# Kernel tuning notes

Measured on AMD Instinct MI355X. Metric: run time of the kernel, lower is better.

Reference implementation:

```python
import jax, jax.numpy as jnp
import numpy as np

N_NODES = 10000
N_EDGES = 80000
IN_DIM = 512
H1, H2, OUT_DIM = 4096, 1024, 7
NEG_SLOPE = 0.2


def _gat_layer(x, src, dst, W, a_src, a_dst, b, n_nodes):
    # x: [N, F_in] -> h: [N, F_out]
    h = x @ W
    # per-edge attention logits: a_src . h_i + a_dst . h_j (PyG GATConv, heads=1)
    e = jax.nn.leaky_relu((h @ a_src)[src] + (h @ a_dst)[dst], NEG_SLOPE)
    # segment softmax over destination nodes
    m = jax.ops.segment_max(e, dst, num_segments=n_nodes)
    ex = jnp.exp(e - m[dst])
    denom = jax.ops.segment_sum(ex, dst, num_segments=n_nodes)
    alpha = ex / denom[dst]
    # scatter-add weighted messages
    out = jax.ops.segment_sum(alpha[:, None] * h[src], dst, num_segments=n_nodes)
    return out + b


def setup_inputs() -> dict:
    key = jax.random.key(0)
    ks = jax.random.split(key, 16)
    s = 0.05
    inp = {
        "x": jax.random.normal(ks[0], (N_NODES, IN_DIM), dtype=jnp.float32),
        "edge_index": jax.random.randint(ks[1], (2, N_EDGES), 0, N_NODES, dtype=jnp.int32),
        "W1": jax.random.normal(ks[2], (IN_DIM, H1), dtype=jnp.float32) * s,
        "att_src1": jax.random.normal(ks[3], (H1,), dtype=jnp.float32) * s,
        "att_dst1": jax.random.normal(ks[4], (H1,), dtype=jnp.float32) * s,
        "b1": jnp.zeros((H1,), dtype=jnp.float32),
        "W2": jax.random.normal(ks[5], (H1, H2), dtype=jnp.float32) * s,
        "att_src2": jax.random.normal(ks[6], (H2,), dtype=jnp.float32) * s,
        "att_dst2": jax.random.normal(ks[7], (H2,), dtype=jnp.float32) * s,
        "b2": jnp.zeros((H2,), dtype=jnp.float32),
        "W3": jax.random.normal(ks[8], (H2, OUT_DIM), dtype=jnp.float32) * s,
        "att_src3": jax.random.normal(ks[9], (OUT_DIM,), dtype=jnp.float32) * s,
        "att_dst3": jax.random.normal(ks[10], (OUT_DIM,), dtype=jnp.float32) * s,
        "b3": jnp.zeros((OUT_DIM,), dtype=jnp.float32),
    }
    return inp


def reference(x, edge_index, W1, att_src1, att_dst1, b1,
              W2, att_src2, att_dst2, b2,
              W3, att_src3, att_dst3, b3):
    n = x.shape[0]
    loops = jnp.arange(n, dtype=edge_index.dtype)
    src = jnp.concatenate([edge_index[0], loops])  # add_self_loops=True
    dst = jnp.concatenate([edge_index[1], loops])
    h = _gat_layer(x, src, dst, W1, att_src1, att_dst1, b1, n)
    h = jax.nn.relu(h)  # dropout is identity in eval mode
    h = _gat_layer(h, src, dst, W2, att_src2, att_dst2, b2, n)
    h = jax.nn.relu(h)
    h = _gat_layer(h, src, dst, W3, att_src3, att_dst3, b3, n)
    return jax.nn.log_softmax(h, axis=1)
```

## Files before the change

### kernel.cpp

```cpp
#include <hip/hip_runtime.h>
#include <hip/hip_bf16.h>
#include <math.h>

#define NNODES  10000
#define NEDGES  80000
#define NTOT    90000
#define IN_DIM  512
#define H1_DIM  4096
#define H2_DIM  1024
#define ODIM    7
#define MAXDEG  128
#define NEG_SLOPE 0.2f
#define MROWS   10240
#define NBX1    (H1_DIM / 128)

typedef __hip_bfloat16 bf16;
typedef __attribute__((ext_vector_type(8))) short short8;
typedef __attribute__((ext_vector_type(4))) float f32x4;

__device__ inline void unpack_bf2(unsigned u, float& lo, float& hi) {
    union { unsigned i; float f; } a, b;
    a.i = u << 16; b.i = u & 0xffff0000u;
    lo = a.f; hi = b.f;
}

#define ASYNC_COPY16(lds, g)                                                              \
    __builtin_amdgcn_global_load_lds((const __attribute__((address_space(1))) void*)(g),  \
                                     (__attribute__((address_space(3))) void*)(lds),      \
                                     16, 0, 0)

__global__ __launch_bounds__(256) void prep_all(const float* __restrict__ W1,
                                                bf16* __restrict__ W1T,
                                                const float* __restrict__ as1,
                                                const float* __restrict__ ad1,
                                                float* __restrict__ w1s,
                                                float* __restrict__ w1d,
                                                const float* __restrict__ W2,
                                                bf16* __restrict__ W2T,
                                                const float* __restrict__ as2,
                                                const float* __restrict__ ad2,
                                                float* __restrict__ w2s,
                                                float* __restrict__ w2d,
                                                const int* __restrict__ ei,
                                                int* cnt, int* bucket) {
    const int nb1 = (H1_DIM / 32) * (IN_DIM / 32);
    const int nb2 = (H2_DIM / 32) * (H1_DIM / 32);
    int bid = blockIdx.x;

    if (bid >= nb1 + nb2) {
        int k = (bid - nb1 - nb2) * 256 + threadIdx.x;
        if (k < NTOT) {
            int s, d;
            if (k < NEDGES) { s = ei[k]; d = ei[NEDGES + k]; }
            else            { s = k - NEDGES; d = s; }
            int pos = atomicAdd(&cnt[d], 1);
            if (pos < MAXDEG) bucket[d * MAXDEG + pos] = s;
        }
        return;
    }

    const float *W, *a_s, *a_d; bf16 *WT; float *w_s, *w_d; int R, C, cblocks;
    if (bid < nb1) { W = W1; WT = W1T; a_s = as1; a_d = ad1; w_s = w1s; w_d = w1d;
                     R = IN_DIM; C = H1_DIM; cblocks = H1_DIM / 32; }
    else { bid -= nb1; W = W2; WT = W2T; a_s = as2; a_d = ad2; w_s = w2s; w_d = w2d;
           R = H1_DIM; C = H2_DIM; cblocks = H2_DIM / 32; }
    int c0 = (bid % cblocks) * 32, r0 = (bid / cblocks) * 32;

    __shared__ float t[32][33];
    int x = threadIdx.x & 31, y = threadIdx.x >> 5;
    float asv = a_s[c0 + x], adv = a_d[c0 + x];
    #pragma unroll
    for (int dy = 0; dy < 32; dy += 8) {
        float w = W[(size_t)(r0 + y + dy) * C + c0 + x];
        t[y + dy][x] = w;
        float ps = w * asv, pd = w * adv;
        #pragma unroll
        for (int off = 16; off > 0; off >>= 1) {
            ps += __shfl_down(ps, off, 32);
            pd += __shfl_down(pd, off, 32);
        }
        if (x == 0) {
            atomicAdd(&w_s[r0 + y + dy], ps);
            atomicAdd(&w_d[r0 + y + dy], pd);
        }
    }
    __syncthreads();
    #pragma unroll
    for (int dy = 0; dy < 32; dy += 8)
        WT[(size_t)(c0 + y + dy) * R + r0 + x] = __float2bfloat16(t[x][y + dy]);
}

__global__ __launch_bounds__(128) void dots_cvt1(const float* __restrict__ X,
                                                 const float* __restrict__ w_s,
                                                 const float* __restrict__ w_d,
                                                 float* __restrict__ s_src,
                                                 float* __restrict__ s_dst,
                                                 bf16* __restrict__ XB) {
    int n = blockIdx.x;
    int t = threadIdx.x;
    float4 xv = ((const float4*)(X + (size_t)n * IN_DIM))[t];
    float4 wsv = ((const float4*)w_s)[t];
    float4 wdv = ((const float4*)w_d)[t];
    bf16 o[4] = { __float2bfloat16(xv.x), __float2bfloat16(xv.y),
                  __float2bfloat16(xv.z), __float2bfloat16(xv.w) };
    *(uint2*)(XB + (size_t)n * IN_DIM + 4 * t) = *(uint2*)o;
    float ss = xv.x*wsv.x + xv.y*wsv.y + xv.z*wsv.z + xv.w*wsv.w;
    float sd = xv.x*wdv.x + xv.y*wdv.y + xv.z*wdv.z + xv.w*wdv.w;
    #pragma unroll
    for (int off = 32; off > 0; off >>= 1) {
        ss += __shfl_down(ss, off);
        sd += __shfl_down(sd, off);
    }
    __shared__ float red[2][2];
    int wave = t >> 6;
    if ((t & 63) == 0) { red[0][wave] = ss; red[1][wave] = sd; }
    __syncthreads();
    if (t == 0) {
        s_src[n] = red[0][0] + red[0][1];
        s_dst[n] = red[1][0] + red[1][1];
    }
}

__global__ __launch_bounds__(128) void agg1(const bf16* __restrict__ XB,
                                            const float* __restrict__ s_src,
                                            const float* __restrict__ s_dst,
                                            const int* __restrict__ bucket,
                                            const int* __restrict__ cnt,
                                            bf16* __restrict__ OUT) {
    int n = blockIdx.x;
    int c = min(cnt[n], MAXDEG);
    __shared__ float alpha[MAXDEG];
    __shared__ int   ssrc[MAXDEG];
    if (threadIdx.x < c) {
        int s = bucket[n * MAXDEG + threadIdx.x];
        ssrc[threadIdx.x] = s;
        float e = s_src[s] + s_dst[n];
        alpha[threadIdx.x] = (e > 0.f) ? e : NEG_SLOPE * e;
    }
    __syncthreads();
    if (threadIdx.x == 0) {
        float m = -1e30f;
        for (int j = 0; j < c; ++j) m = fmaxf(m, alpha[j]);
        float s = 0.f;
        for (int j = 0; j < c; ++j) { float ex = __expf(alpha[j] - m); alpha[j] = ex; s += ex; }
        float inv = 1.f / s;
        for (int j = 0; j < c; ++j) alpha[j] *= inv;
    }
    __syncthreads();
    int t = threadIdx.x;
    float acc[4] = {};
    for (int j = 0; j < c; ++j) {
        float a = alpha[j];
        uint2 raw = ((const uint2*)(XB + (size_t)ssrc[j] * IN_DIM))[t];
        float f0, f1, f2, f3;
        unpack_bf2(raw.x, f0, f1); unpack_bf2(raw.y, f2, f3);
        acc[0] = fmaf(a, f0, acc[0]); acc[1] = fmaf(a, f1, acc[1]);
        acc[2] = fmaf(a, f2, acc[2]); acc[3] = fmaf(a, f3, acc[3]);
    }
    bf16 o[4] = { __float2bfloat16(acc[0]), __float2bfloat16(acc[1]),
                  __float2bfloat16(acc[2]), __float2bfloat16(acc[3]) };
    *(uint2*)(OUT + (size_t)n * IN_DIM + 4 * t) = *(uint2*)o;
}

__global__ __launch_bounds__(256) void reduce_dots(const float* __restrict__ ps,
                                                   const float* __restrict__ pd,
                                                   float* __restrict__ s_src,
                                                   float* __restrict__ s_dst) {
    int g = blockIdx.x * 256 + threadIdx.x;
    if (g >= NNODES) return;
    float s = 0.f, d = 0.f;
    #pragma unroll
    for (int b = 0; b < NBX1; ++b) {
        s += ps[(size_t)b * MROWS + g];
        d += pd[(size_t)b * MROWS + g];
    }
    s_src[g] = s; s_dst[g] = d;
}

__global__ __launch_bounds__(128) void agg2_h3(const bf16* __restrict__ H,
                                               const float* __restrict__ s_src,
                                               const float* __restrict__ s_dst,
                                               const int* __restrict__ bucket,
                                               const int* __restrict__ cnt,
                                               const float* __restrict__ bias,
                                               const float* __restrict__ W3,
                                               const float* __restrict__ as3,
                                               const float* __restrict__ ad3,
                                               float* __restrict__ H3,
                                               float* __restrict__ s3_src,
                                               float* __restrict__ s3_dst) {
    int n = blockIdx.x;
    int c = min(cnt[n], MAXDEG);
    __shared__ float alpha[MAXDEG];
    __shared__ int   ssrc[MAXDEG];
    if (threadIdx.x < c) {
        int s = bucket[n * MAXDEG + threadIdx.x];
        ssrc[threadIdx.x] = s;
        float e = s_src[s] + s_dst[n];
        alpha[threadIdx.x] = (e > 0.f) ? e : NEG_SLOPE * e;
    }
    __syncthreads();
    if (threadIdx.x == 0) {
        float m = -1e30f;
        for (int j = 0; j < c; ++j) m = fmaxf(m, alpha[j]);
        float s = 0.f;
        for (int j = 0; j < c; ++j) { float ex = __expf(alpha[j] - m); alpha[j] = ex; s += ex; }
        float inv = 1.f / s;
        for (int j = 0; j < c; ++j) alpha[j] *= inv;
    }
    __syncthreads();
    int t = threadIdx.x;
    float acc[8] = {};
    for (int j = 0; j < c; ++j) {
        float a = alpha[j];
        uint4 raw = ((const uint4*)(H + (size_t)ssrc[j] * H2_DIM))[t];
        float f0, f1, f2, f3, f4, f5, f6, f7;
        unpack_bf2(raw.x, f0, f1); unpack_bf2(raw.y, f2, f3);
        unpack_bf2(raw.z, f4, f5); unpack_bf2(raw.w, f6, f7);
        acc[0] = fmaf(a, f0, acc[0]); acc[1] = fmaf(a, f1, acc[1]);
        acc[2] = fmaf(a, f2, acc[2]); acc[3] = fmaf(a, f3, acc[3]);
        acc[4] = fmaf(a, f4, acc[4]); acc[5] = fmaf(a, f5, acc[5]);
        acc[6] = fmaf(a, f6, acc[6]); acc[7] = fmaf(a, f7, acc[7]);
    }
    float p[ODIM] = {};
    #pragma unroll
    for (int k = 0; k < 8; ++k) {
        float v = fmaxf(acc[k] + bias[8 * t + k], 0.f);
        const float* wrow = W3 + (size_t)(8 * t + k) * ODIM;
        #pragma unroll
        for (int o = 0; o < ODIM; ++o)
            p[o] = fmaf(v, wrow[o], p[o]);
    }
    #pragma unroll
    for (int o = 0; o < ODIM; ++o)
        #pragma unroll
        for (int off = 32; off > 0; off >>= 1)
            p[o] += __shfl_down(p[o], off);
    __shared__ float red[2][ODIM];
    int wave = t >> 6;
    if ((t & 63) == 0)
        #pragma unroll
        for (int o = 0; o < ODIM; ++o) red[wave][o] = p[o];
    __syncthreads();
    if (t == 0) {
        float ss = 0.f, sd = 0.f;
        #pragma unroll
        for (int o = 0; o < ODIM; ++o) {
            float v = red[0][o] + red[1][o];
            H3[n * ODIM + o] = v;
            ss = fmaf(v, as3[o], ss);
            sd = fmaf(v, ad3[o], sd);
        }
        s3_src[n] = ss; s3_dst[n] = sd;
    }
}

template<bool BIASRELU, bool FUSEDOTS, bool PIPE>
__global__ __launch_bounds__(256) void gemm_mfma(const bf16* __restrict__ A,
                                                 const bf16* __restrict__ BT,
                                                 const float* __restrict__ bias,
                                                 const float* __restrict__ w_s,
                                                 const float* __restrict__ w_d,
                                                 float* __restrict__ s_src,
                                                 float* __restrict__ s_dst,
                                                 bf16* __restrict__ C,
                                                 int M, int N, int K) {
    constexpr int TM = 128, TN = 128, NI = 4, NJ = 4;
    __shared__ alignas(16) bf16 As[2][TM][32];
    __shared__ alignas(16) bf16 Bs[2][TN][32];
    __shared__ float pd_s[FUSEDOTS ? TM : 1];
    __shared__ float pd_d[FUSEDOTS ? TM : 1];
    const int tid  = threadIdx.x;
    const int wave = tid >> 6;
    const int lane = tid & 63;

    const int gx = gridDim.x;
    const int j  = blockIdx.y * gx + blockIdx.x;
    const int band = j / (8 * gx);
    const int r8   = j - band * (8 * gx);
    const int by = (r8 & 7) + 8 * band;
    const int bx = r8 >> 3;
    const int row0 = by * TM;
    const int col0 = bx * TN;
    if (row0 >= M) return;

    if constexpr (FUSEDOTS) {
        if (tid < TM) { pd_s[tid] = 0.f; pd_d[tid] = 0.f; }
    }

    const int wr0 = (wave >> 1) * 64;
    const int wc0 = (wave & 1) * 64;

    const int srow  = tid >> 2;
    const int skoff = ((tid & 3) ^ (srow & 3)) * 8;
    const bf16* a0 = A + (size_t)min(row0 + srow, M - 1) * K + skoff;
    const bf16* a1 = A + (size_t)min(row0 + 64 + srow, M - 1) * K + skoff;
    const bf16* b0 = BT + (size_t)(col0 + srow) * K + skoff;
    const bf16* b1 = BT + (size_t)(col0 + 64 + srow) * K + skoff;

    f32x4 acc[NI][NJ] = {};
    const int fRow  = lane & 15;
    const int fKoff = ((lane >> 4) ^ (fRow & 3)) * 8;

    if constexpr (PIPE) {
        const int NIT = K >> 5;
        ASYNC_COPY16(&As[0][wave * 16][0],      a0);
        ASYNC_COPY16(&As[0][64 + wave * 16][0], a1);
        ASYNC_COPY16(&Bs[0][wave * 16][0],      b0);
        ASYNC_COPY16(&Bs[0][64 + wave * 16][0], b1);
        __syncthreads();
        for (int it = 0; it < NIT; ++it) {
            const int cb = it & 1, nb = cb ^ 1;
            if (it + 1 < NIT) {
                const int ko = (it + 1) << 5;
                ASYNC_COPY16(&As[nb][wave * 16][0],      a0 + ko);
                ASYNC_COPY16(&As[nb][64 + wave * 16][0], a1 + ko);
                ASYNC_COPY16(&Bs[nb][wave * 16][0],      b0 + ko);
                ASYNC_COPY16(&Bs[nb][64 + wave * 16][0], b1 + ko);
            }
            short8 af[NI], bfr[NJ];
            #pragma unroll
            for (int i = 0; i < NI; ++i)
                af[i] = *(const short8*)&As[cb][wr0 + i * 16 + fRow][fKoff];
            #pragma unroll
            for (int jj = 0; jj < NJ; ++jj)
                bfr[jj] = *(const short8*)&Bs[cb][wc0 + jj * 16 + fRow][fKoff];
            #pragma unroll
            for (int i = 0; i < NI; ++i)
                #pragma unroll
                for (int jj = 0; jj < NJ; ++jj)
                    acc[i][jj] = __builtin_amdgcn_mfma_f32_16x16x32_bf16(af[i], bfr[jj], acc[i][jj], 0, 0, 0);
            __syncthreads();
        }
    } else {
        for (int k0 = 0; k0 < K; k0 += 64) {
            #pragma unroll
            for (int h = 0; h < 2; ++h) {
                ASYNC_COPY16(&As[h][wave * 16][0],      a0 + k0 + h * 32);
                ASYNC_COPY16(&As[h][64 + wave * 16][0], a1 + k0 + h * 32);
                ASYNC_COPY16(&Bs[h][wave * 16][0],      b0 + k0 + h * 32);
                ASYNC_COPY16(&Bs[h][64 + wave * 16][0], b1 + k0 + h * 32);
            }
            __syncthreads();
            #pragma unroll
            for (int h = 0; h < 2; ++h) {
                short8 af[NI], bfr[NJ];
                #pragma unroll
                for (int i = 0; i < NI; ++i)
                    af[i] = *(const short8*)&As[h][wr0 + i * 16 + fRow][fKoff];
                #pragma unroll
                for (int jj = 0; jj < NJ; ++jj)
                    bfr[jj] = *(const short8*)&Bs[h][wc0 + jj * 16 + fRow][fKoff];
                #pragma unroll
                for (int i = 0; i < NI; ++i)
                    #pragma unroll
                    for (int jj = 0; jj < NJ; ++jj)
                        acc[i][jj] = __builtin_amdgcn_mfma_f32_16x16x32_bf16(af[i], bfr[jj], acc[i][jj], 0, 0, 0);
            }
            __syncthreads();
        }
    }

    const int crow = (lane >> 4) * 4;
    const int ccol = lane & 15;
    #pragma unroll
    for (int i = 0; i < NI; ++i) {
        #pragma unroll
        for (int r = 0; r < 4; ++r) {
            int gm = row0 + wr0 + i * 16 + crow + r;
            float vss = 0.f, vsd = 0.f;
            if (gm < M) {
                #pragma unroll
                for (int jj = 0; jj < NJ; ++jj) {
                    int gn = col0 + wc0 + jj * 16 + ccol;
                    float v = acc[i][jj][r];
                    if (BIASRELU) v = fmaxf(v + bias[gn], 0.f);
                    C[(size_t)gm * N + gn] = __float2bfloat16(v);
                    if (FUSEDOTS) {
                        vss = fmaf(v, w_s[gn], vss);
                        vsd = fmaf(v, w_d[gn], vsd);
                    }
                }
            }
            if (FUSEDOTS) {
                #pragma unroll
                for (int m2 = 1; m2 < 16; m2 <<= 1) {
                    vss += __shfl_xor(vss, m2, 16);
                    vsd += __shfl_xor(vsd, m2, 16);
                }
                if ((lane & 15) == 0) {
                    atomicAdd(&pd_s[wr0 + i * 16 + crow + r], vss);
                    atomicAdd(&pd_d[wr0 + i * 16 + crow + r], vsd);
                }
            }
        }
    }
    if constexpr (FUSEDOTS) {
        __syncthreads();
        if (tid < TM) {
            s_src[(size_t)bx * MROWS + row0 + tid] = pd_s[tid];
            s_dst[(size_t)bx * MROWS + row0 + tid] = pd_d[tid];
        }
    }
}

__global__ __launch_bounds__(128) void aggregate3(const float* __restrict__ H3,
                                                  const float* __restrict__ s_src,
                                                  const float* __restrict__ s_dst,
                                                  const int* __restrict__ bucket,
                                                  const int* __restrict__ cnt,
                                                  const float* __restrict__ b3,
                                                  float* __restrict__ out) {
    int n = blockIdx.x;
    int c = min(cnt[n], MAXDEG);
    __shared__ float alpha[MAXDEG];
    __shared__ int   ssrc[MAXDEG];
    __shared__ float o[ODIM];
    if (threadIdx.x < c) {
        int s = bucket[n * MAXDEG + threadIdx.x];
        ssrc[threadIdx.x] = s;
        float e = s_src[s] + s_dst[n];
        alpha[threadIdx.x] = (e > 0.f) ? e : NEG_SLOPE * e;
    }
    __syncthreads();
    if (threadIdx.x == 0) {
        float m = -1e30f;
        for (int j = 0; j < c; ++j) m = fmaxf(m, alpha[j]);
        float s = 0.f;
        for (int j = 0; j < c; ++j) { float ex = __expf(alpha[j] - m); alpha[j] = ex; s += ex; }
        float inv = 1.f / s;
        for (int j = 0; j < c; ++j) alpha[j] *= inv;
    }
    __syncthreads();
    if (threadIdx.x < ODIM) {
        float acc = 0.f;
        for (int j = 0; j < c; ++j)
            acc = fmaf(alpha[j], H3[ssrc[j] * ODIM + threadIdx.x], acc);
        o[threadIdx.x] = acc + b3[threadIdx.x];
    }
    __syncthreads();
    if (threadIdx.x == 0) {
        float m = o[0];
        for (int k = 1; k < ODIM; ++k) m = fmaxf(m, o[k]);
        float s = 0.f;
        for (int k = 0; k < ODIM; ++k) s += __expf(o[k] - m);
        float lse = m + logf(s);
        for (int k = 0; k < ODIM; ++k) out[n * ODIM + k] = o[k] - lse;
    }
}

extern "C" void kernel_launch(void* const* d_in, const int* in_sizes, int n_in,
                              void* d_out, int out_size, void* d_ws, size_t ws_size,
                              hipStream_t stream) {
    const float* x   = (const float*)d_in[0];
    const int*   ei  = (const int*)  d_in[1];
    const float* W1  = (const float*)d_in[2];
    const float* as1 = (const float*)d_in[3];
    const float* ad1 = (const float*)d_in[4];
    const float* b1  = (const float*)d_in[5];
    const float* W2  = (const float*)d_in[6];
    const float* as2 = (const float*)d_in[7];
    const float* ad2 = (const float*)d_in[8];
    const float* b2  = (const float*)d_in[9];
    const float* W3  = (const float*)d_in[10];
    const float* as3 = (const float*)d_in[11];
    const float* ad3 = (const float*)d_in[12];
    const float* b3  = (const float*)d_in[13];
    float* outp = (float*)d_out;

    char* p = (char*)d_ws;
    bf16*  x2     = (bf16*)p;   p += (size_t)NNODES * H1_DIM * sizeof(bf16);
    bf16*  r2     = (bf16*)p;   p += (size_t)NNODES * H2_DIM * sizeof(bf16);
    bf16*  r3     = (bf16*)p;   p += (size_t)NNODES * H2_DIM * sizeof(bf16);
    bf16*  W2T    = (bf16*)p;   p += (size_t)H2_DIM * H1_DIM * sizeof(bf16);
    float* pds    = (float*)p;  p += (size_t)NBX1 * MROWS * sizeof(float);
    float* pdd    = (float*)p;  p += (size_t)NBX1 * MROWS * sizeof(float);
    float* h3     = (float*)p;  p += (size_t)NNODES * ODIM * sizeof(float);
    float* ssrc   = (float*)p;  p += NNODES * sizeof(float);
    float* sdst   = (float*)p;  p += NNODES * sizeof(float);
    float* ssrc3  = (float*)p;  p += NNODES * sizeof(float);
    float* sdst3  = (float*)p;  p += NNODES * sizeof(float);
    float* w1s    = (float*)p;  p += IN_DIM * sizeof(float);
    float* w1d    = (float*)p;  p += IN_DIM * sizeof(float);
    float* w2s    = (float*)p;  p += H1_DIM * sizeof(float);
    float* w2d    = (float*)p;  p += H1_DIM * sizeof(float);
    int*   cnt    = (int*)p;    p += NNODES * sizeof(int);
    int*   bucket = (int*)p;    p += (size_t)NNODES * MAXDEG * sizeof(int);
    size_t required = (size_t)(p - (char*)d_ws);
    if (ws_size < required) return;

    bf16* xb    = x2;
    bf16* aggxb = r2;
    bf16* h2    = r2;
    bf16* W1T   = r3;

    hipMemsetAsync(cnt, 0, NNODES * sizeof(int), stream);
    hipMemsetAsync(w1s, 0, (2 * IN_DIM + 2 * H1_DIM) * sizeof(float), stream);

    {
        int nb1 = (H1_DIM / 32) * (IN_DIM / 32);
        int nb2 = (H2_DIM / 32) * (H1_DIM / 32);
        int nbB = (NTOT + 255) / 256;
        prep_all<<<nb1 + nb2 + nbB, 256, 0, stream>>>(W1, W1T, as1, ad1, w1s, w1d,
                                                      W2, W2T, as2, ad2, w2s, w2d,
                                                      ei, cnt, bucket);
    }

    dots_cvt1<<<NNODES, 128, 0, stream>>>(x, w1s, w1d, ssrc, sdst, xb);
    agg1<<<NNODES, 128, 0, stream>>>(xb, ssrc, sdst, bucket, cnt, aggxb);

    const int nRowPad = ((((NNODES + 127) / 128) + 7) / 8) * 8;

    {
        dim3 g(H1_DIM / 128, nRowPad);
        gemm_mfma<true, true, false><<<g, 256, 0, stream>>>(aggxb, W1T, b1, w2s, w2d,
                                                            pds, pdd, x2, NNODES, H1_DIM, IN_DIM);
    }
    reduce_dots<<<(NNODES + 255) / 256, 256, 0, stream>>>(pds, pdd, ssrc, sdst);

    {
        dim3 g(H2_DIM / 128, nRowPad);
        gemm_mfma<false, false, true><<<g, 256, 0, stream>>>(x2, W2T, nullptr, nullptr, nullptr,
                                                             nullptr, nullptr, h2, NNODES, H2_DIM, H1_DIM);
    }

    agg2_h3<<<NNODES, 128, 0, stream>>>(h2, ssrc, sdst, bucket, cnt, b2,
                                        W3, as3, ad3, h3, ssrc3, sdst3);

    aggregate3<<<NNODES, 128, 0, stream>>>(h3, ssrc3, sdst3, bucket, cnt, b3, outp);
}
```

Baseline: 429.0 us.

## Merge small per-node kernels into cooperative kernels with grid syncs

Replaces the separate dots/agg1 launches with one cooperative kernel, and reduce_dots/agg2_h3/aggregate3 with another. Each uses a fixed grid of 1024 blocks, grid-stride loops over nodes and grid.sync() between phases. This removes several kernel launches and their gaps, at the cost of grid-wide barriers and a persistent grid that may expose less parallelism than one block per node.

After: 853.3 us. 1.99x slower.

```diff
diff --git a/kernel.cpp b/kernel.cpp
--- a/kernel.cpp
+++ b/kernel.cpp
@@ -1,6 +1,9 @@
 #include <hip/hip_runtime.h>
 #include <hip/hip_bf16.h>
+#include <hip/hip_cooperative_groups.h>
 #include <math.h>
+
+namespace cg = cooperative_groups;
 
 #define NNODES  10000
 #define NEDGES  80000
@@ -13,6 +16,7 @@
 #define NEG_SLOPE 0.2f
 #define MROWS   10240
 #define NBX1    (H1_DIM / 128)
+#define COOPB   1024
 
 typedef __hip_bfloat16 bf16;
 typedef __attribute__((ext_vector_type(8))) short short8;
@@ -90,168 +94,79 @@
         WT[(size_t)(c0 + y + dy) * R + r0 + x] = __float2bfloat16(t[x][y + dy]);
 }
 
-__global__ __launch_bounds__(128) void dots_cvt1(const float* __restrict__ X,
-                                                 const float* __restrict__ w_s,
-                                                 const float* __restrict__ w_d,
-                                                 float* __restrict__ s_src,
-                                                 float* __restrict__ s_dst,
-                                                 bf16* __restrict__ XB) {
-    int n = blockIdx.x;
-    int t = threadIdx.x;
-    float4 xv = ((const float4*)(X + (size_t)n * IN_DIM))[t];
-    float4 wsv = ((const float4*)w_s)[t];
-    float4 wdv = ((const float4*)w_d)[t];
-    bf16 o[4] = { __float2bfloat16(xv.x), __float2bfloat16(xv.y),
-                  __float2bfloat16(xv.z), __float2bfloat16(xv.w) };
-    *(uint2*)(XB + (size_t)n * IN_DIM + 4 * t) = *(uint2*)o;
-    float ss = xv.x*wsv.x + xv.y*wsv.y + xv.z*wsv.z + xv.w*wsv.w;
-    float sd = xv.x*wdv.x + xv.y*wdv.y + xv.z*wdv.z + xv.w*wdv.w;
-    #pragma unroll
-    for (int off = 32; off > 0; off >>= 1) {
-        ss += __shfl_down(ss, off);
-        sd += __shfl_down(sd, off);
-    }
+__global__ __launch_bounds__(128) void layer1_coop(const float* __restrict__ X,
+                                                   const float* __restrict__ w_s,
+                                                   const float* __restrict__ w_d,
+                                                   float* __restrict__ s_src,
+                                                   float* __restrict__ s_dst,
+                                                   bf16* __restrict__ XB,
+                                                   const int* __restrict__ bucket,
+                                                   const int* __restrict__ cnt,
+                                                   bf16* __restrict__ OUT) {
+    cg::grid_group grid = cg::this_grid();
     __shared__ float red[2][2];
-    int wave = t >> 6;
-    if ((t & 63) == 0) { red[0][wave] = ss; red[1][wave] = sd; }
-    __syncthreads();
-    if (t == 0) {
-        s_src[n] = red[0][0] + red[0][1];
-        s_dst[n] = red[1][0] + red[1][1];
-    }
-}
-
-__global__ __launch_bounds__(128) void agg1(const bf16* __restrict__ XB,
-                                            const float* __restrict__ s_src,
-                                            const float* __restrict__ s_dst,
-                                            const int* __restrict__ bucket,
-                                            const int* __restrict__ cnt,
-                                            bf16* __restrict__ OUT) {
-    int n = blockIdx.x;
-    int c = min(cnt[n], MAXDEG);
     __shared__ float alpha[MAXDEG];
     __shared__ int   ssrc[MAXDEG];
-    if (threadIdx.x < c) {
-        int s = bucket[n * MAXDEG + threadIdx.x];
-        ssrc[threadIdx.x] = s;
-        float e = s_src[s] + s_dst[n];
-        alpha[threadIdx.x] = (e > 0.f) ? e : NEG_SLOPE * e;
-    }
-    __syncthreads();
-    if (threadIdx.x == 0) {
-        float m = -1e30f;
-        for (int j = 0; j < c; ++j) m = fmaxf(m, alpha[j]);
-        float s = 0.f;
-        for (int j = 0; j < c; ++j) { float ex = __expf(alpha[j] - m); alpha[j] = ex; s += ex; }
-        float inv = 1.f / s;
-        for (int j = 0; j < c; ++j) alpha[j] *= inv;
-    }
-    __syncthreads();
-    int t = threadIdx.x;
-    float acc[4] = {};
-    for (int j = 0; j < c; ++j) {
-        float a = alpha[j];
-        uint2 raw = ((const uint2*)(XB + (size_t)ssrc[j] * IN_DIM))[t];
-        float f0, f1, f2, f3;
-        unpack_bf2(raw.x, f0, f1); unpack_bf2(raw.y, f2, f3);
-        acc[0] = fmaf(a, f0, acc[0]); acc[1] = fmaf(a, f1, acc[1]);
-        acc[2] = fmaf(a, f2, acc[2]); acc[3] = fmaf(a, f3, acc[3]);
-    }
-    bf16 o[4] = { __float2bfloat16(acc[0]), __float2bfloat16(acc[1]),
-                  __float2bfloat16(acc[2]), __float2bfloat16(acc[3]) };
-    *(uint2*)(OUT + (size_t)n * IN_DIM + 4 * t) = *(uint2*)o;
-}
-
-__global__ __launch_bounds__(256) void reduce_dots(const float* __restrict__ ps,
-                                                   const float* __restrict__ pd,
-                                                   float* __restrict__ s_src,
-                                                   float* __restrict__ s_dst) {
-    int g = blockIdx.x * 256 + threadIdx.x;
-    if (g >= NNODES) return;
-    float s = 0.f, d = 0.f;
-    #pragma unroll
-    for (int b = 0; b < NBX1; ++b) {
-        s += ps[(size_t)b * MROWS + g];
-        d += pd[(size_t)b * MROWS + g];
-    }
-    s_src[g] = s; s_dst[g] = d;
-}
-
-__global__ __launch_bounds__(128) void agg2_h3(const bf16* __restrict__ H,
-                                               const float* __restrict__ s_src,
-                                               const float* __restrict__ s_dst,
-                                               const int* __restrict__ bucket,
-                                               const int* __restrict__ cnt,
-                                               const float* __restrict__ bias,
-                                               const float* __restrict__ W3,
-                                               const float* __restrict__ as3,
-                                               const float* __restrict__ ad3,
-                                               float* __restrict__ H3,
-                                               float* __restrict__ s3_src,
-                                               float* __restrict__ s3_dst) {
-    int n = blockIdx.x;
-    int c = min(cnt[n], MAXDEG);
-    __shared__ float alpha[MAXDEG];
-    __shared__ int   ssrc[MAXDEG];
-    if (threadIdx.x < c) {
-        int s = bucket[n * MAXDEG + threadIdx.x];
-        ssrc[threadIdx.x] = s;
-        float e = s_src[s] + s_dst[n];
-        alpha[threadIdx.x] = (e > 0.f) ? e : NEG_SLOPE * e;
-    }
-    __syncthreads();
-    if (threadIdx.x == 0) {
-        float m = -1e30f;
-        for (int j = 0; j < c; ++j) m = fmaxf(m, alpha[j]);
-        float s = 0.f;
-        for (int j = 0; j < c; ++j) { float ex = __expf(alpha[j] - m); alpha[j] = ex; s += ex; }
-        float inv = 1.f / s;
-        for (int j = 0; j < c; ++j) alpha[j] *= inv;
-    }
-    __syncthreads();
-    int t = threadIdx.x;
-    float acc[8] = {};
-    for (int j = 0; j < c; ++j) {
-        float a = alpha[j];
-        uint4 raw = ((const uint4*)(H + (size_t)ssrc[j] * H2_DIM))[t];
-        float f0, f1, f2, f3, f4, f5, f6, f7;
-        unpack_bf2(raw.x, f0, f1); unpack_bf2(raw.y, f2, f3);
-        unpack_bf2(raw.z, f4, f5); unpack_bf2(raw.w, f6, f7);
-        acc[0] = fmaf(a, f0, acc[0]); acc[1] = fmaf(a, f1, acc[1]);
-        acc[2] = fmaf(a, f2, acc[2]); acc[3] = fmaf(a, f3, acc[3]);
-        acc[4] = fmaf(a, f4, acc[4]); acc[5] = fmaf(a, f5, acc[5]);
-        acc[6] = fmaf(a, f6, acc[6]); acc[7] = fmaf(a, f7, acc[7]);
-    }
-    float p[ODIM] = {};
-    #pragma unroll
-    for (int k = 0; k < 8; ++k) {
-        float v = fmaxf(acc[k] + bias[8 * t + k], 0.f);
-        const float* wrow = W3 + (size_t)(8 * t + k) * ODIM;
+    const int t = threadIdx.x;
+    const int wave = t >> 6;
+
+    for (int n = blockIdx.x; n < NNODES; n += gridDim.x) {
+        float4 xv = ((const float4*)(X + (size_t)n * IN_DIM))[t];
+        float4 wsv = ((const float4*)w_s)[t];
+        float4 wdv = ((const float4*)w_d)[t];
+        bf16 o[4] = { __float2bfloat16(xv.x), __float2bfloat16(xv.y),
+                      __float2bfloat16(xv.z), __float2bfloat16(xv.w) };
+        *(uint2*)(XB + (size_t)n * IN_DIM + 4 * t) = *(uint2*)o;
+        float ss = xv.x*wsv.x + xv.y*wsv.y + xv.z*wsv.z + xv.w*wsv.w;
+        float sd = xv.x*wdv.x + xv.y*wdv.y + xv.z*wdv.z + xv.w*wdv.w;
         #pragma unroll
-        for (int o = 0; o < ODIM; ++o)
-            p[o] = fmaf(v, wrow[o], p[o]);
-    }
-    #pragma unroll
-    for (int o = 0; o < ODIM; ++o)
-        #pragma unroll
-        for (int off = 32; off > 0; off >>= 1)
-            p[o] += __shfl_down(p[o], off);
-    __shared__ float red[2][ODIM];
-    int wave = t >> 6;
-    if ((t & 63) == 0)
-        #pragma unroll
-        for (int o = 0; o < ODIM; ++o) red[wave][o] = p[o];
-    __syncthreads();
-    if (t == 0) {
-        float ss = 0.f, sd = 0.f;
-        #pragma unroll
-        for (int o = 0; o < ODIM; ++o) {
-            float v = red[0][o] + red[1][o];
-            H3[n * ODIM + o] = v;
-            ss = fmaf(v, as3[o], ss);
-            sd = fmaf(v, ad3[o], sd);
-        }
-        s3_src[n] = ss; s3_dst[n] = sd;
+        for (int off = 32; off > 0; off >>= 1) {
+            ss += __shfl_down(ss, off);
+            sd += __shfl_down(sd, off);
+        }
+        if ((t & 63) == 0) { red[0][wave] = ss; red[1][wave] = sd; }
+        __syncthreads();
+        if (t == 0) {
+            s_src[n] = red[0][0] + red[0][1];
+            s_dst[n] = red[1][0] + red[1][1];
+        }
+        __syncthreads();
+    }
+
+    __threadfence();
+    grid.sync();
+
+    for (int n = blockIdx.x; n < NNODES; n += gridDim.x) {
+        int c = min(cnt[n], MAXDEG);
+        if (t < c) {
+            int s = bucket[n * MAXDEG + t];
+            ssrc[t] = s;
+            float e = s_src[s] + s_dst[n];
+            alpha[t] = (e > 0.f) ? e : NEG_SLOPE * e;
+        }
+        __syncthreads();
+        if (t == 0) {
+            float m = -1e30f;
+            for (int j = 0; j < c; ++j) m = fmaxf(m, alpha[j]);
+            float s = 0.f;
+            for (int j = 0; j < c; ++j) { float ex = __expf(alpha[j] - m); alpha[j] = ex; s += ex; }
+            float inv = 1.f / s;
+            for (int j = 0; j < c; ++j) alpha[j] *= inv;
+        }
+        __syncthreads();
+        float acc[4] = {};
+        for (int j = 0; j < c; ++j) {
+            float a = alpha[j];
+            uint2 raw = ((const uint2*)(XB + (size_t)ssrc[j] * IN_DIM))[t];
+            float f0, f1, f2, f3;
+            unpack_bf2(raw.x, f0, f1); unpack_bf2(raw.y, f2, f3);
+            acc[0] = fmaf(a, f0, acc[0]); acc[1] = fmaf(a, f1, acc[1]);
+            acc[2] = fmaf(a, f2, acc[2]); acc[3] = fmaf(a, f3, acc[3]);
+        }
+        bf16 o[4] = { __float2bfloat16(acc[0]), __float2bfloat16(acc[1]),
+                      __float2bfloat16(acc[2]), __float2bfloat16(acc[3]) };
+        *(uint2*)(OUT + (size_t)n * IN_DIM + 4 * t) = *(uint2*)o;
+        __syncthreads();
     }
 }
 
@@ -404,48 +319,140 @@
     }
 }
 
-__global__ __launch_bounds__(128) void aggregate3(const float* __restrict__ H3,
-                                                  const float* __restrict__ s_src,
-                                                  const float* __restrict__ s_dst,
-                                                  const int* __restrict__ bucket,
-                                                  const int* __restrict__ cnt,
-                                                  const float* __restrict__ b3,
-                                                  float* __restrict__ out) {
-    int n = blockIdx.x;
-    int c = min(cnt[n], MAXDEG);
+__global__ __launch_bounds__(128) void layer3_coop(const float* __restrict__ pds,
+                                                   const float* __restrict__ pdd,
+                                                   float* __restrict__ s_src,
+                                                   float* __restrict__ s_dst,
+                                                   const bf16* __restrict__ H,
+                                                   const int* __restrict__ bucket,
+                                                   const int* __restrict__ cnt,
+                                                   const float* __restrict__ bias,
+                                                   const float* __restrict__ W3,
+                                                   const float* __restrict__ as3,
+                                                   const float* __restrict__ ad3,
+                                                   float* __restrict__ H3,
+                                                   float* __restrict__ s3_src,
+                                                   float* __restrict__ s3_dst,
+                                                   const float* __restrict__ b3,
+                                                   float* __restrict__ out) {
+    cg::grid_group grid = cg::this_grid();
     __shared__ float alpha[MAXDEG];
     __shared__ int   ssrc[MAXDEG];
-    __shared__ float o[ODIM];
-    if (threadIdx.x < c) {
-        int s = bucket[n * MAXDEG + threadIdx.x];
-        ssrc[threadIdx.x] = s;
-        float e = s_src[s] + s_dst[n];
-        alpha[threadIdx.x] = (e > 0.f) ? e : NEG_SLOPE * e;
-    }
-    __syncthreads();
-    if (threadIdx.x == 0) {
-        float m = -1e30f;
-        for (int j = 0; j < c; ++j) m = fmaxf(m, alpha[j]);
-        float s = 0.f;
-        for (int j = 0; j < c; ++j) { float ex = __expf(alpha[j] - m); alpha[j] = ex; s += ex; }
-        float inv = 1.f / s;
-        for (int j = 0; j < c; ++j) alpha[j] *= inv;
-    }
-    __syncthreads();
-    if (threadIdx.x < ODIM) {
-        float acc = 0.f;
-        for (int j = 0; j < c; ++j)
-            acc = fmaf(alpha[j], H3[ssrc[j] * ODIM + threadIdx.x], acc);
-        o[threadIdx.x] = acc + b3[threadIdx.x];
-    }
-    __syncthreads();
-    if (threadIdx.x == 0) {
-        float m = o[0];
-        for (int k = 1; k < ODIM; ++k) m = fmaxf(m, o[k]);
-        float s = 0.f;
-        for (int k = 0; k < ODIM; ++k) s += __expf(o[k] - m);
-        float lse = m + logf(s);
-        for (int k = 0; k < ODIM; ++k) out[n * ODIM + k] = o[k] - lse;
+    __shared__ float red[2][ODIM];
+    __shared__ float ovec[ODIM];
+    const int t = threadIdx.x;
+    const int wave = t >> 6;
+
+    for (int g = blockIdx.x * 128 + t; g < NNODES; g += gridDim.x * 128) {
+        float s = 0.f, d = 0.f;
+        #pragma unroll
+        for (int b = 0; b < NBX1; ++b) {
+            s += pds[(size_t)b * MROWS + g];
+            d += pdd[(size_t)b * MROWS + g];
+        }
+        s_src[g] = s; s_dst[g] = d;
+    }
+    __threadfence();
+    grid.sync();
+
+    for (int n = blockIdx.x; n < NNODES; n += gridDim.x) {
+        int c = min(cnt[n], MAXDEG);
+        if (t < c) {
+            int s = bucket[n * MAXDEG + t];
+            ssrc[t] = s;
+            float e = s_src[s] + s_dst[n];
+            alpha[t] = (e > 0.f) ? e : NEG_SLOPE * e;
+        }
+        __syncthreads();
+        if (t == 0) {
+            float m = -1e30f;
+            for (int j = 0; j < c; ++j) m = fmaxf(m, alpha[j]);
+            float s = 0.f;
+            for (int j = 0; j < c; ++j) { float ex = __expf(alpha[j] - m); alpha[j] = ex; s += ex; }
+            float inv = 1.f / s;
+            for (int j = 0; j < c; ++j) alpha[j] *= inv;
+        }
+        __syncthreads();
+        float acc[8] = {};
+        for (int j = 0; j < c; ++j) {
+            float a = alpha[j];
+            uint4 raw = ((const uint4*)(H + (size_t)ssrc[j] * H2_DIM))[t];
+            float f0, f1, f2, f3, f4, f5, f6, f7;
+            unpack_bf2(raw.x, f0, f1); unpack_bf2(raw.y, f2, f3);
+            unpack_bf2(raw.z, f4, f5); unpack_bf2(raw.w, f6, f7);
+            acc[0] = fmaf(a, f0, acc[0]); acc[1] = fmaf(a, f1, acc[1]);
+            acc[2] = fmaf(a, f2, acc[2]); acc[3] = fmaf(a, f3, acc[3]);
+            acc[4] = fmaf(a, f4, acc[4]); acc[5] = fmaf(a, f5, acc[5]);
+            acc[6] = fmaf(a, f6, acc[6]); acc[7] = fmaf(a, f7, acc[7]);
+        }
+        float p[ODIM] = {};
+        #pragma unroll
+        for (int k = 0; k < 8; ++k) {
+            float v = fmaxf(acc[k] + bias[8 * t + k], 0.f);
+            const float* wrow = W3 + (size_t)(8 * t + k) * ODIM;
+            #pragma unroll
+            for (int o = 0; o < ODIM; ++o)
+                p[o] = fmaf(v, wrow[o], p[o]);
+        }
+        #pragma unroll
+        for (int o = 0; o < ODIM; ++o)
+            #pragma unroll
+            for (int off = 32; off > 0; off >>= 1)
+                p[o] += __shfl_down(p[o], off);
+        if ((t & 63) == 0)
+            #pragma unroll
+            for (int o = 0; o < ODIM; ++o) red[wave][o] = p[o];
+        __syncthreads();
+        if (t == 0) {
+            float ss = 0.f, sd = 0.f;
+            #pragma unroll
+            for (int o = 0; o < ODIM; ++o) {
+                float v = red[0][o] + red[1][o];
+                H3[n * ODIM + o] = v;
+                ss = fmaf(v, as3[o], ss);
+                sd = fmaf(v, ad3[o], sd);
+            }
+            s3_src[n] = ss; s3_dst[n] = sd;
+        }
+        __syncthreads();
+    }
+    __threadfence();
+    grid.sync();
+
+    for (int n = blockIdx.x; n < NNODES; n += gridDim.x) {
+        int c = min(cnt[n], MAXDEG);
+        if (t < c) {
+            int s = bucket[n * MAXDEG + t];
+            ssrc[t] = s;
+            float e = s3_src[s] + s3_dst[n];
+            alpha[t] = (e > 0.f) ? e : NEG_SLOPE * e;
+        }
+        __syncthreads();
+        if (t == 0) {
+            float m = -1e30f;
+            for (int j = 0; j < c; ++j) m = fmaxf(m, alpha[j]);
+            float s = 0.f;
+            for (int j = 0; j < c; ++j) { float ex = __expf(alpha[j] - m); alpha[j] = ex; s += ex; }
+            float inv = 1.f / s;
+            for (int j = 0; j < c; ++j) alpha[j] *= inv;
+        }
+        __syncthreads();
+        if (t < ODIM) {
+            float acc = 0.f;
+            for (int j = 0; j < c; ++j)
+                acc = fmaf(alpha[j], H3[ssrc[j] * ODIM + t], acc);
+            ovec[t] = acc + b3[t];
+        }
+        __syncthreads();
+        if (t == 0) {
+            float m = ovec[0];
+            for (int k = 1; k < ODIM; ++k) m = fmaxf(m, ovec[k]);
+            float s = 0.f;
+            for (int k = 0; k < ODIM; ++k) s += __expf(ovec[k] - m);
+            float lse = m + logf(s);
+            for (int k = 0; k < ODIM; ++k) out[n * ODIM + k] = ovec[k] - lse;
+        }
+        __syncthreads();
     }
 }
 
@@ -506,8 +513,11 @@
                                                       ei, cnt, bucket);
     }
 
-    dots_cvt1<<<NNODES, 128, 0, stream>>>(x, w1s, w1d, ssrc, sdst, xb);
-    agg1<<<NNODES, 128, 0, stream>>>(xb, ssrc, sdst, bucket, cnt, aggxb);
+    {
+        void* args[] = { (void*)&x, (void*)&w1s, (void*)&w1d, (void*)&ssrc, (void*)&sdst,
+                         (void*)&xb, (void*)&bucket, (void*)&cnt, (void*)&aggxb };
+        hipLaunchCooperativeKernel((void*)layer1_coop, dim3(COOPB), dim3(128), args, 0, stream);
+    }
 
     const int nRowPad = ((((NNODES + 127) / 128) + 7) / 8) * 8;
 
@@ -516,7 +526,6 @@
         gemm_mfma<true, true, false><<<g, 256, 0, stream>>>(aggxb, W1T, b1, w2s, w2d,
                                                             pds, pdd, x2, NNODES, H1_DIM, IN_DIM);
     }
-    reduce_dots<<<(NNODES + 255) / 256, 256, 0, stream>>>(pds, pdd, ssrc, sdst);
 
     {
         dim3 g(H2_DIM / 128, nRowPad);
@@ -524,8 +533,11 @@
                                                              nullptr, nullptr, h2, NNODES, H2_DIM, H1_DIM);
     }
 
-    agg2_h3<<<NNODES, 128, 0, stream>>>(h2, ssrc, sdst, bucket, cnt, b2,
-                                        W3, as3, ad3, h3, ssrc3, sdst3);
-
-    aggregate3<<<NNODES, 128, 0, stream>>>(h3, ssrc3, sdst3, bucket, cnt, b3, outp);
+    {
+        void* args[] = { (void*)&pds, (void*)&pdd, (void*)&ssrc, (void*)&sdst, (void*)&h2,
+                         (void*)&bucket, (void*)&cnt, (void*)&b2, (void*)&W3, (void*)&as3,
+                         (void*)&ad3, (void*)&h3, (void*)&ssrc3, (void*)&sdst3, (void*)&b3,
+                         (void*)&outp };
+        hipLaunchCooperativeKernel((void*)layer3_coop, dim3(COOPB), dim3(128), args, 0, stream);
+    }
 }
```
